# Kernel optimization log

Measured on AMD Instinct MI355X. Metric: run time of the kernel, lower is better.

## Reference

```python
import jax, jax.numpy as jnp
import numpy as np

IN_FEATURES = 8192
OUT_FEATURES = 8192
NNZ = 671088  # in*out*(1-0.99)
BATCH = 1024


def setup_inputs() -> dict:
    key = jax.random.key(0)
    kx, kv, kr, kc = jax.random.split(key, 4)
    x = jax.random.normal(kx, (BATCH, IN_FEATURES), dtype=jnp.float32)
    # values initialized ~ N(0,1) / sqrt(in_features), matching the module
    values = jax.random.normal(kv, (NNZ,), dtype=jnp.float32) * (1.0 / np.sqrt(IN_FEATURES))
    bias = jnp.zeros((OUT_FEATURES,), dtype=jnp.float32)
    rows = jax.random.randint(kr, (NNZ,), 0, IN_FEATURES, dtype=jnp.int32)
    cols = jax.random.randint(kc, (NNZ,), 0, OUT_FEATURES, dtype=jnp.int32)
    return {"x": x, "values": values, "bias": bias, "rows": rows, "cols": cols}


def reference(x, values, bias, rows, cols):
    # Materialize the sparse (in, out) weight via scatter-add.
    # Duplicate (row, col) pairs sum, matching torch COO .coalesce().
    W = jnp.zeros((IN_FEATURES, OUT_FEATURES), dtype=values.dtype)
    W = W.at[rows, cols].add(values)
    # res = addmm(bias, x, W) == x @ W + bias
    return x @ W + bias[None, :]
```

## Files before the change

kernel.cpp:

```cpp
#include <hip/hip_runtime.h>
#include <stdint.h>

#define IN_F   8192
#define OUT_F  8192
#define BATCH  1024
#define BT     8
#define NBT    (BATCH / BT)
#define MAIN_THREADS 1024
#define GROUPS_PER_WAVE 4
#define L_PREF 160
#define XTILE_BYTES (IN_F * 16)

#define NBUCKET 1024
#define P1_THREADS 1024
#define P1_PER 4
#define P1_CHUNK (P1_THREADS * P1_PER)
#define P2_THREADS 1024
#define BIN_STRIDE (L_PREF + 1)

#if __has_builtin(__builtin_amdgcn_fdot2) && __has_builtin(__builtin_amdgcn_perm)
#define USE_DOT2 1
typedef _Float16 half2v __attribute__((ext_vector_type(2)));
#else
#define USE_DOT2 0
#endif

typedef float f32x2 __attribute__((ext_vector_type(2)));


__device__ __forceinline__ unsigned f32_to_bf16_bits_rne(float f) {
    union { float f; unsigned u; } v; v.f = f;
    unsigned u = v.u;
    unsigned r = u + 0x7FFFu + ((u >> 16) & 1u);
    return r >> 16;
}
__device__ __forceinline__ float bf16_hi_bits_to_f32(unsigned b) {
    union { unsigned u; float f; } v; v.u = b & 0xFFFF0000u; return v.f;
}
__device__ __forceinline__ f32x2 unpack_pair(unsigned u) {
    union { unsigned u; float f; } lo, hi;
    lo.u = u << 16; hi.u = u & 0xFFFF0000u;
    f32x2 r; r.x = lo.f; r.y = hi.f; return r;
}

#if USE_DOT2
__device__ __forceinline__ unsigned val_bits(float f) {
    return (unsigned)__builtin_bit_cast(unsigned short, (_Float16)f);
}
__device__ __forceinline__ unsigned x_bits(float f) {
    return (unsigned)__builtin_bit_cast(unsigned short, (_Float16)f);
}
#else
__device__ __forceinline__ unsigned val_bits(float f) { return f32_to_bf16_bits_rne(f); }
__device__ __forceinline__ unsigned x_bits(float f)   { return f32_to_bf16_bits_rne(f); }
#endif

__global__ __launch_bounds__(P1_THREADS) void bin_kernel(
        const int* __restrict__ rows, const int* __restrict__ cols,
        const float* __restrict__ vals,
        int* __restrict__ bcnt, unsigned* __restrict__ ell, int nnz, int L) {
    __shared__ int lcnt[NBUCKET];
    __shared__ int lbase[NBUCKET];
    __shared__ int gbase[NBUCKET];
    __shared__ int wsum[16];
    __shared__ unsigned stage[P1_CHUNK];
    __shared__ unsigned short smap[P1_CHUNK];

    int tid = threadIdx.x;
    int i0 = blockIdx.x * P1_CHUNK;
    lcnt[tid] = 0;
    __syncthreads();

    unsigned mypk[P1_PER];
    int      myb[P1_PER];
    int      myrk[P1_PER];
#pragma unroll
    for (int k = 0; k < P1_PER; ++k) {
        int i = i0 + k * P1_THREADS + tid;
        myb[k] = -1;
        mypk[k] = 0;
        myrk[k] = 0;
        if (i < nnz) {
            int c = cols[i];
            mypk[k] = (val_bits(vals[i]) << 16) | ((unsigned)rows[i] << 3) | ((unsigned)c & 7u);
            myb[k] = c >> 3;
            myrk[k] = atomicAdd(&lcnt[c >> 3], 1);
        }
    }
    __syncthreads();

    {
        int wv = tid >> 6, ln = tid & 63;
        int v = lcnt[tid];
        int sc = v;
#pragma unroll
        for (int off = 1; off < 64; off <<= 1) {
            int o = __shfl_up(sc, off, 64);
            if (ln >= off) sc += o;
        }
        if (ln == 63) wsum[wv] = sc;
        __syncthreads();
        if (tid < 16) {
            int s = wsum[tid];
            int sl = s;
#pragma unroll
            for (int off = 1; off < 16; off <<= 1) {
                int o = __shfl_up(sl, off, 16);
                if (tid >= off) sl += o;
            }
            wsum[tid] = sl - s;
        }
        __syncthreads();
        lbase[tid] = sc - v + wsum[wv];
    }
    __syncthreads();

    {
        int lc = lcnt[tid];
        gbase[tid] = lc ? atomicAdd(&bcnt[tid], lc) : 0;
    }
#pragma unroll
    for (int k = 0; k < P1_PER; ++k) {
        if (myb[k] >= 0) {
            int pos = lbase[myb[k]] + myrk[k];
            stage[pos] = mypk[k];
            smap[pos] = (unsigned short)myb[k];
        }
    }
    __syncthreads();

    int total = lbase[NBUCKET - 1] + lcnt[NBUCKET - 1];
    int cap = 8 * L;
    for (int i = tid; i < total; i += P1_THREADS) {
        int b = smap[i];
        int idx = gbase[b] + (i - lbase[b]);
        if (idx < cap)
            ell[(size_t)b * cap + idx] = stage[i];
    }
}

__global__ __launch_bounds__(P2_THREADS) void build_kernel(
        const int* __restrict__ bcnt, unsigned* __restrict__ ell,
        int* __restrict__ counts, int L) {
    __shared__ unsigned bins[64 * BIN_STRIDE];
    __shared__ int scnt[64 * 8];
    __shared__ int soff[64 * 8];
    __shared__ int qsh;
    int g = blockIdx.x;
    int tid = threadIdx.x;
    for (int i = tid; i < 64 * BIN_STRIDE; i += P2_THREADS) bins[i] = 0;
    if (tid < 512) scnt[tid] = 0;
    __syncthreads();

    unsigned* slab = ell + (size_t)g * (64 * L);
    int cap = 8 * L;

#pragma unroll 1
    for (int q = 0; q < 8; ++q) {
        int cb = bcnt[g * 8 + q];
        if (cb > cap) cb = cap;
        const unsigned* bp = slab + q * cap;
        for (int i = tid; i < cb; i += P2_THREADS) {
            unsigned e = bp[i];
            int c64 = q * 8 + (int)(e & 7u);
            int sb = (int)((e >> 3) & 7u);
            atomicAdd(&scnt[c64 * 8 + sb], 1);
        }
    }
    __syncthreads();

    if (tid < 64) {
        int rot = tid & 7;
        int off = 0;
#pragma unroll
        for (int k = 0; k < 8; ++k) {
            int sb = (k + rot) & 7;
            soff[tid * 8 + sb] = off;
            off += scnt[tid * 8 + sb];
        }
        counts[g * 64 + tid] = off;
        int mc = min(off, L);
#pragma unroll
        for (int o = 32; o; o >>= 1) mc = max(mc, __shfl_xor(mc, o, 64));
        if (tid == 0) qsh = (mc + 3) >> 2;
#pragma unroll
        for (int k = 0; k < 8; ++k) scnt[tid * 8 + k] = 0;
    }
    __syncthreads();

#pragma unroll 1
    for (int q = 0; q < 8; ++q) {
        int cb = bcnt[g * 8 + q];
        if (cb > cap) cb = cap;
        const unsigned* bp = slab + q * cap;
        for (int i = tid; i < cb; i += P2_THREADS) {
            unsigned e = bp[i];
            int c64 = q * 8 + (int)(e & 7u);
            int sb = (int)((e >> 3) & 7u);
            int rk = atomicAdd(&scnt[c64 * 8 + sb], 1);
            int pos = soff[c64 * 8 + sb] + rk;
            if (pos < L) bins[c64 * BIN_STRIDE + pos] = e;
        }
    }
    __syncthreads();

    int D = qsh << 8;
    for (int d = tid; d < D; d += P2_THREADS) {
        int q = d >> 8, r = d & 255;
        slab[d] = bins[(r >> 2) * BIN_STRIDE + q * 4 + (r & 3)];
    }
}

#if USE_DOT2
__device__ __forceinline__ void process_pair8(unsigned pk0, unsigned pk1, const char* xbase,
        float& a0, float& a1, float& a2, float& a3,
        float& a4, float& a5, float& a6, float& a7) {
    unsigned off0 = pk0 & 0xFFF8u;
    unsigned off1 = pk1 & 0xFFF8u;
    uint4 q0 = *(const uint4*)(xbase + off0 * 2);
    uint4 q1 = *(const uint4*)(xbase + off1 * 2);
    unsigned vv = __builtin_amdgcn_perm(pk1, pk0, 0x07060302u);
    half2v vh = __builtin_bit_cast(half2v, vv);
    unsigned e0 = __builtin_amdgcn_perm(q1.x, q0.x, 0x05040100u);
    unsigned o0 = __builtin_amdgcn_perm(q1.x, q0.x, 0x07060302u);
    unsigned e1 = __builtin_amdgcn_perm(q1.y, q0.y, 0x05040100u);
    unsigned o1 = __builtin_amdgcn_perm(q1.y, q0.y, 0x07060302u);
    unsigned e2 = __builtin_amdgcn_perm(q1.z, q0.z, 0x05040100u);
    unsigned o2 = __builtin_amdgcn_perm(q1.z, q0.z, 0x07060302u);
    unsigned e3 = __builtin_amdgcn_perm(q1.w, q0.w, 0x05040100u);
    unsigned o3 = __builtin_amdgcn_perm(q1.w, q0.w, 0x07060302u);
    a0 = __builtin_amdgcn_fdot2(__builtin_bit_cast(half2v, e0), vh, a0, false);
    a1 = __builtin_amdgcn_fdot2(__builtin_bit_cast(half2v, o0), vh, a1, false);
    a2 = __builtin_amdgcn_fdot2(__builtin_bit_cast(half2v, e1), vh, a2, false);
    a3 = __builtin_amdgcn_fdot2(__builtin_bit_cast(half2v, o1), vh, a3, false);
    a4 = __builtin_amdgcn_fdot2(__builtin_bit_cast(half2v, e2), vh, a4, false);
    a5 = __builtin_amdgcn_fdot2(__builtin_bit_cast(half2v, o2), vh, a5, false);
    a6 = __builtin_amdgcn_fdot2(__builtin_bit_cast(half2v, e3), vh, a6, false);
    a7 = __builtin_amdgcn_fdot2(__builtin_bit_cast(half2v, o3), vh, a7, false);
}
#else
__device__ __forceinline__ void process_entry8(unsigned pk, const char* xbase,
                                               f32x2& a01, f32x2& a23, f32x2& a45, f32x2& a67) {
    float val = bf16_hi_bits_to_f32(pk);
    f32x2 vv; vv.x = val; vv.y = val;
    unsigned off = pk & 0xFFF8u;
    uint4 d = *(const uint4*)(xbase + off * 2);
    a01 = __builtin_elementwise_fma(unpack_pair(d.x), vv, a01);
    a23 = __builtin_elementwise_fma(unpack_pair(d.y), vv, a23);
    a45 = __builtin_elementwise_fma(unpack_pair(d.z), vv, a45);
    a67 = __builtin_elementwise_fma(unpack_pair(d.w), vv, a67);
}
#endif

__global__ __launch_bounds__(MAIN_THREADS) void spmm_kernel(
        const float* __restrict__ x,
        const float* __restrict__ bias,
        const int* __restrict__ counts,
        const unsigned* __restrict__ ell,
        float* __restrict__ out, int L) {
    extern __shared__ uint4 xl[];
    int w = blockIdx.x;
    int bt = w >> 1;
    int half = w & 1;
    int t = threadIdx.x;
    int b0 = bt * BT;

    for (int r = t; r < IN_F; r += MAIN_THREADS) {
        unsigned u0 = x_bits(x[(b0 + 0) * IN_F + r]);
        unsigned u1 = x_bits(x[(b0 + 1) * IN_F + r]);
        unsigned u2 = x_bits(x[(b0 + 2) * IN_F + r]);
        unsigned u3 = x_bits(x[(b0 + 3) * IN_F + r]);
        unsigned u4 = x_bits(x[(b0 + 4) * IN_F + r]);
        unsigned u5 = x_bits(x[(b0 + 5) * IN_F + r]);
        unsigned u6 = x_bits(x[(b0 + 6) * IN_F + r]);
        unsigned u7 = x_bits(x[(b0 + 7) * IN_F + r]);
        uint4 d;
        d.x = (u1 << 16) | u0;
        d.y = (u3 << 16) | u2;
        d.z = (u5 << 16) | u4;
        d.w = (u7 << 16) | u6;
        xl[r] = d;
    }
    __syncthreads();

    const char* xbase = (const char*)xl;
    int wave = t >> 6;
    int lane = t & 63;
    int n4cap = L >> 2;

#pragma unroll 1
    for (int it = 0; it < GROUPS_PER_WAVE; ++it) {
        int g = half * 64 + wave * GROUPS_PER_WAVE + it;
        int col = (g << 6) + lane;
        int cnt = counts[col];
#pragma unroll
        for (int off = 32; off; off >>= 1) cnt = max(cnt, __shfl_xor(cnt, off, 64));
        int n4 = (cnt + 3) >> 2;
        n4 = min(n4, n4cap);
        const uint4* ep = (const uint4*)(ell + (size_t)g * (L * 64));
        float bv = bias[col];
#if USE_DOT2
        float a0 = 0.f, a1 = 0.f, a2 = 0.f, a3 = 0.f;
        float a4 = 0.f, a5 = 0.f, a6 = 0.f, a7 = 0.f;
        if (n4 > 0) {
            uint4 q = ep[lane];
#pragma unroll 1
            for (int s4 = 1; s4 < n4; ++s4) {
                uint4 qn = ep[s4 * 64 + lane];
                process_pair8(q.x, q.y, xbase, a0, a1, a2, a3, a4, a5, a6, a7);
                process_pair8(q.z, q.w, xbase, a0, a1, a2, a3, a4, a5, a6, a7);
                q = qn;
            }
            process_pair8(q.x, q.y, xbase, a0, a1, a2, a3, a4, a5, a6, a7);
            process_pair8(q.z, q.w, xbase, a0, a1, a2, a3, a4, a5, a6, a7);
        }
        out[(size_t)(b0 + 0) * OUT_F + col] = a0 + bv;
        out[(size_t)(b0 + 1) * OUT_F + col] = a1 + bv;
        out[(size_t)(b0 + 2) * OUT_F + col] = a2 + bv;
        out[(size_t)(b0 + 3) * OUT_F + col] = a3 + bv;
        out[(size_t)(b0 + 4) * OUT_F + col] = a4 + bv;
        out[(size_t)(b0 + 5) * OUT_F + col] = a5 + bv;
        out[(size_t)(b0 + 6) * OUT_F + col] = a6 + bv;
        out[(size_t)(b0 + 7) * OUT_F + col] = a7 + bv;
#else
        f32x2 a01 = {0.f, 0.f}, a23 = {0.f, 0.f}, a45 = {0.f, 0.f}, a67 = {0.f, 0.f};
        if (n4 > 0) {
            uint4 q = ep[lane];
#pragma unroll 1
            for (int s4 = 1; s4 < n4; ++s4) {
                uint4 qn = ep[s4 * 64 + lane];
                process_entry8(q.x, xbase, a01, a23, a45, a67);
                process_entry8(q.y, xbase, a01, a23, a45, a67);
                process_entry8(q.z, xbase, a01, a23, a45, a67);
                process_entry8(q.w, xbase, a01, a23, a45, a67);
                q = qn;
            }
            process_entry8(q.x, xbase, a01, a23, a45, a67);
            process_entry8(q.y, xbase, a01, a23, a45, a67);
            process_entry8(q.z, xbase, a01, a23, a45, a67);
            process_entry8(q.w, xbase, a01, a23, a45, a67);
        }
        out[(size_t)(b0 + 0) * OUT_F + col] = a01.x + bv;
        out[(size_t)(b0 + 1) * OUT_F + col] = a01.y + bv;
        out[(size_t)(b0 + 2) * OUT_F + col] = a23.x + bv;
        out[(size_t)(b0 + 3) * OUT_F + col] = a23.y + bv;
        out[(size_t)(b0 + 4) * OUT_F + col] = a45.x + bv;
        out[(size_t)(b0 + 5) * OUT_F + col] = a45.y + bv;
        out[(size_t)(b0 + 6) * OUT_F + col] = a67.x + bv;
        out[(size_t)(b0 + 7) * OUT_F + col] = a67.y + bv;
#endif
    }
}

extern "C" void kernel_launch(void* const* d_in, const int* in_sizes, int n_in,
                              void* d_out, int out_size, void* d_ws, size_t ws_size,
                              hipStream_t stream) {
    const float* x      = (const float*)d_in[0];
    const float* values = (const float*)d_in[1];
    const float* bias   = (const float*)d_in[2];
    const int* rows = (const int*)d_in[3];
    const int* cols = (const int*)d_in[4];
    float* out = (float*)d_out;
    int nnz = in_sizes[1];

    int* bcnt   = (int*)d_ws;
    int* counts = bcnt + NBUCKET;
    unsigned* ell = (unsigned*)(counts + 8192);

    long long cap_slots = ((long long)(ws_size / 4) - (NBUCKET + 8192)) / 8192;
    int L = (int)(cap_slots & ~3LL);
    if (L > L_PREF) L = L_PREF;
    if (L < 4) L = 4;

    static int attr_set = -1;
    if (attr_set < 0) {
        hipFuncSetAttribute((const void*)spmm_kernel,
                            hipFuncAttributeMaxDynamicSharedMemorySize, XTILE_BYTES);
        attr_set = 1;
    }

    hipMemsetAsync(bcnt, 0, NBUCKET * 4, stream);
    int nb1 = (nnz + P1_CHUNK - 1) / P1_CHUNK;
    bin_kernel<<<nb1, P1_THREADS, 0, stream>>>(rows, cols, values, bcnt, ell, nnz, L);
    build_kernel<<<128, P2_THREADS, 0, stream>>>(bcnt, ell, counts, L);
    spmm_kernel<<<NBT * 2, MAIN_THREADS, XTILE_BYTES, stream>>>(x, bias, counts, ell, out, L);
}
```

Baseline: 163.1 us.

## Software-pipeline LDS gathers two stages ahead and hoist counts/bias loads

Splits each entry step into separate LDS gather loads and dot-product compute, then double-buffers two groups of four entries so the x gathers for later entries are in flight while earlier ones are being accumulated. It also moves the per-group count reduction and bias loads ahead of the x tile staging so their global latency overlaps with that work. The aim is to hide LDS load latency in the inner loop, at the cost of more live registers, which could lower occupancy.

```diff
diff --git a/kernel.cpp b/kernel.cpp
--- a/kernel.cpp
+++ b/kernel.cpp
@@ -212,13 +212,13 @@
 }
 
 #if USE_DOT2
-__device__ __forceinline__ void process_pair8(unsigned pk0, unsigned pk1, const char* xbase,
+__device__ __forceinline__ uint4 ld_x16(const char* xbase, unsigned pk) {
+    unsigned off = pk & 0xFFF8u;
+    return *(const uint4*)(xbase + off * 2);
+}
+__device__ __forceinline__ void dot_pair(unsigned pk0, unsigned pk1, uint4 q0, uint4 q1,
         float& a0, float& a1, float& a2, float& a3,
         float& a4, float& a5, float& a6, float& a7) {
-    unsigned off0 = pk0 & 0xFFF8u;
-    unsigned off1 = pk1 & 0xFFF8u;
-    uint4 q0 = *(const uint4*)(xbase + off0 * 2);
-    uint4 q1 = *(const uint4*)(xbase + off1 * 2);
     unsigned vv = __builtin_amdgcn_perm(pk1, pk0, 0x07060302u);
     half2v vh = __builtin_bit_cast(half2v, vv);
     unsigned e0 = __builtin_amdgcn_perm(q1.x, q0.x, 0x05040100u);
@@ -238,6 +238,13 @@
     a6 = __builtin_amdgcn_fdot2(__builtin_bit_cast(half2v, e3), vh, a6, false);
     a7 = __builtin_amdgcn_fdot2(__builtin_bit_cast(half2v, o3), vh, a7, false);
 }
+#define DOTQ(q, x0, x1, x2, x3) \
+    do { dot_pair((q).x, (q).y, (x0), (x1), a0, a1, a2, a3, a4, a5, a6, a7); \
+         dot_pair((q).z, (q).w, (x2), (x3), a0, a1, a2, a3, a4, a5, a6, a7); } while (0)
+#define LD4A(q) do { xA0 = ld_x16(xbase, (q).x); xA1 = ld_x16(xbase, (q).y); \
+                     xA2 = ld_x16(xbase, (q).z); xA3 = ld_x16(xbase, (q).w); } while (0)
+#define LD4B(q) do { xB0 = ld_x16(xbase, (q).x); xB1 = ld_x16(xbase, (q).y); \
+                     xB2 = ld_x16(xbase, (q).z); xB3 = ld_x16(xbase, (q).w); } while (0)
 #else
 __device__ __forceinline__ void process_entry8(unsigned pk, const char* xbase,
                                                f32x2& a01, f32x2& a23, f32x2& a45, f32x2& a67) {
@@ -264,6 +271,23 @@
     int half = w & 1;
     int t = threadIdx.x;
     int b0 = bt * BT;
+    int wave = t >> 6;
+    int lane = t & 63;
+    int n4cap = L >> 2;
+
+    int   n44[GROUPS_PER_WAVE];
+    float bv4[GROUPS_PER_WAVE];
+#pragma unroll
+    for (int it = 0; it < GROUPS_PER_WAVE; ++it) {
+        int g = half * 64 + wave * GROUPS_PER_WAVE + it;
+        int col = (g << 6) + lane;
+        int cnt = counts[col];
+#pragma unroll
+        for (int off = 32; off; off >>= 1) cnt = max(cnt, __shfl_xor(cnt, off, 64));
+        int n4 = (cnt + 3) >> 2;
+        n44[it] = min(n4, n4cap);
+        bv4[it] = bias[col];
+    }
 
     for (int r = t; r < IN_F; r += MAIN_THREADS) {
         unsigned u0 = x_bits(x[(b0 + 0) * IN_F + r]);
@@ -284,35 +308,50 @@
     __syncthreads();
 
     const char* xbase = (const char*)xl;
-    int wave = t >> 6;
-    int lane = t & 63;
-    int n4cap = L >> 2;
 
 #pragma unroll 1
     for (int it = 0; it < GROUPS_PER_WAVE; ++it) {
         int g = half * 64 + wave * GROUPS_PER_WAVE + it;
         int col = (g << 6) + lane;
-        int cnt = counts[col];
-#pragma unroll
-        for (int off = 32; off; off >>= 1) cnt = max(cnt, __shfl_xor(cnt, off, 64));
-        int n4 = (cnt + 3) >> 2;
-        n4 = min(n4, n4cap);
+        int n4 = n44[it];
         const uint4* ep = (const uint4*)(ell + (size_t)g * (L * 64));
-        float bv = bias[col];
+        float bv = bv4[it];
 #if USE_DOT2
         float a0 = 0.f, a1 = 0.f, a2 = 0.f, a3 = 0.f;
         float a4 = 0.f, a5 = 0.f, a6 = 0.f, a7 = 0.f;
         if (n4 > 0) {
-            uint4 q = ep[lane];
+            uint4 qA = ep[lane];
+            uint4 xA0, xA1, xA2, xA3;
+            LD4A(qA);
+            uint4 qB;
+            uint4 xB0, xB1, xB2, xB3;
+            if (n4 > 1) {
+                qB = ep[64 + lane];
+                LD4B(qB);
+            }
+            int s4 = 2;
 #pragma unroll 1
-            for (int s4 = 1; s4 < n4; ++s4) {
-                uint4 qn = ep[s4 * 64 + lane];
-                process_pair8(q.x, q.y, xbase, a0, a1, a2, a3, a4, a5, a6, a7);
-                process_pair8(q.z, q.w, xbase, a0, a1, a2, a3, a4, a5, a6, a7);
-                q = qn;
+            for (; s4 + 1 < n4; s4 += 2) {
+                uint4 qC = ep[s4 * 64 + lane];
+                uint4 qD = ep[(s4 + 1) * 64 + lane];
+                DOTQ(qA, xA0, xA1, xA2, xA3);
+                qA = qC;
+                LD4A(qA);
+                DOTQ(qB, xB0, xB1, xB2, xB3);
+                qB = qD;
+                LD4B(qB);
             }
-            process_pair8(q.x, q.y, xbase, a0, a1, a2, a3, a4, a5, a6, a7);
-            process_pair8(q.z, q.w, xbase, a0, a1, a2, a3, a4, a5, a6, a7);
+            if (s4 < n4) {
+                uint4 qC = ep[s4 * 64 + lane];
+                DOTQ(qA, xA0, xA1, xA2, xA3);
+                qA = qC;
+                LD4A(qA);
+                DOTQ(qB, xB0, xB1, xB2, xB3);
+                DOTQ(qA, xA0, xA1, xA2, xA3);
+            } else {
+                DOTQ(qA, xA0, xA1, xA2, xA3);
+                if (n4 > 1) DOTQ(qB, xB0, xB1, xB2, xB3);
+            }
         }
         out[(size_t)(b0 + 0) * OUT_F + col] = a0 + bv;
         out[(size_t)(b0 + 1) * OUT_F + col] = a1 + bv;
```

After: 159.2 us. -2.4%, faster.
